# Performance work log

Measured on AMD Instinct MI355X. Metric: run time of the kernel, lower is better.

The kernel has to match this reference:

```python
import jax, jax.numpy as jnp
import numpy as np

LOWER = 300  # hidden size of the critic MLP


def setup_inputs() -> dict:
    key = jax.random.key(0)
    ks = jax.random.split(key, 6)
    N, XD, YD = 1024, 768, 768
    x = jax.random.normal(ks[0], (N, XD), dtype=jnp.float32)
    y = jax.random.normal(ks[1], (N, YD), dtype=jnp.float32)
    # Linear(x_dim+y_dim -> LOWER), Linear(LOWER -> 1); Kaiming-uniform-ish init
    b1_lim = 1.0 / np.sqrt(XD + YD)
    b2_lim = 1.0 / np.sqrt(LOWER)
    W1 = jax.random.uniform(ks[2], (XD + YD, LOWER), jnp.float32, -b1_lim, b1_lim)
    b1 = jax.random.uniform(ks[3], (LOWER,), jnp.float32, -b1_lim, b1_lim)
    W2 = jax.random.uniform(ks[4], (LOWER, 1), jnp.float32, -b2_lim, b2_lim)
    b2 = jax.random.uniform(ks[5], (1,), jnp.float32, -b2_lim, b2_lim)
    return {"x_samples": x, "y_samples": y, "W1": W1, "b1": b1, "W2": W2, "b2": b2}


def reference(x_samples, y_samples, W1, b1, W2, b2):
    N = y_samples.shape[0]
    xd = x_samples.shape[-1]
    # Decompose first Linear: cat([x, y]) @ W1 == x @ W1[:xd] + y @ W1[xd:]
    Wx, Wy = W1[:xd], W1[xd:]
    hx = x_samples @ Wx          # [N, LOWER]
    hy = y_samples @ Wy          # [N, LOWER]
    w2 = W2[:, 0]                # [LOWER]

    def critic(h):
        # relu -> Linear(LOWER->1) -> softplus
        return jax.nn.softplus(jax.nn.relu(h) @ w2 + b2[0])

    # T0[i] = F(x[i], y[i])
    T0 = critic(hx + hy + b1)                       # [N]
    # T1[i, j] = F(x[j], y[i])  (x tiled over dim 0, y over dim 1)
    h_pair = hy[:, None, :] + hx[None, :, :] + b1   # [N, N, LOWER]
    T1 = critic(h_pair)                             # [N, N]
    lower_bound = (T0.mean()
                   - jax.nn.logsumexp(T1, axis=1).mean()
                   - jnp.log(jnp.float32(N)))
    return lower_bound
```

## Files before the change

kernel.cpp:

```cpp
#include <hip/hip_runtime.h>
#include <math.h>

#define N_S 1024
#define XD  768
#define LOW 300
#define KP  320
#define KP2 160

typedef _Float16 h2  __attribute__((ext_vector_type(2)));
typedef __fp16   g2  __attribute__((ext_vector_type(2)));
typedef _Float16 v8h __attribute__((ext_vector_type(8)));
typedef float    f4  __attribute__((ext_vector_type(4)));

union U32H2 { unsigned int u; h2 h; };
__device__ inline h2 u2h(unsigned int v){ U32H2 t; t.u = v; return t.h; }
__device__ inline unsigned int pk(float a, float b){
    g2 t = __builtin_amdgcn_cvt_pkrtz(a, b);
    return __builtin_bit_cast(unsigned int, t);
}
union U4V8 { uint4 u; v8h v; };

__global__ __launch_bounds__(256)
void gemm_h(const float* __restrict__ x, const float* __restrict__ y,
            const float* __restrict__ W1, const float* __restrict__ b1g,
            unsigned int* __restrict__ hx_h, unsigned int* __restrict__ hy_h)
{
    __shared__ unsigned int As[2][32][34];
    __shared__ unsigned int Bs[2][64][34];

    const int tid = threadIdx.x;
    const int job = blockIdx.x;
    const int which = job >= 160;
    const int t = which ? job - 160 : job;
    const int n0 = (t % 5) * 64;
    const int r0 = (t / 5) * 32;
    const float* A = which ? y : x;
    const float* W = W1 + (size_t)which * XD * LOW;
    _Float16* outh = (_Float16*)(which ? hy_h : hx_h);

    const int w = tid >> 6, l = tid & 63;
    const int wn = w & 1, wm = w >> 1;
    const int lr = l & 15, lg = l >> 4;

    const int arow = tid >> 3, aq = tid & 7;
    const int bn = tid & 63, bms = tid >> 6;
    const bool bin = (n0 + bn) < LOW;

    f4 acc[2] = {};
    float4 a0, a1; float bw[16];
    a0 = *(const float4*)&A[(size_t)(r0 + arow) * XD + aq * 8];
    a1 = *(const float4*)&A[(size_t)(r0 + arow) * XD + aq * 8 + 4];
    #pragma unroll
    for (int s = 0; s < 16; ++s)
        bw[s] = bin ? W[(size_t)(bms * 16 + s) * LOW + n0 + bn] : 0.f;

    const int NC = XD / 64;
    for (int c = 0; c < NC; ++c) {
        const int buf = c & 1;
        *(uint4*)&As[buf][arow][aq * 4] =
            uint4{ pk(a0.x,a0.y), pk(a0.z,a0.w), pk(a1.x,a1.y), pk(a1.z,a1.w) };
        *(uint4*)&Bs[buf][bn][bms * 8] =
            uint4{ pk(bw[0],bw[1]), pk(bw[2],bw[3]), pk(bw[4],bw[5]), pk(bw[6],bw[7]) };
        *(uint4*)&Bs[buf][bn][bms * 8 + 4] =
            uint4{ pk(bw[8],bw[9]), pk(bw[10],bw[11]), pk(bw[12],bw[13]), pk(bw[14],bw[15]) };
        __syncthreads();
        if (c + 1 < NC) {
            const int kb = (c + 1) * 64;
            a0 = *(const float4*)&A[(size_t)(r0 + arow) * XD + kb + aq * 8];
            a1 = *(const float4*)&A[(size_t)(r0 + arow) * XD + kb + aq * 8 + 4];
            #pragma unroll
            for (int s = 0; s < 16; ++s)
                bw[s] = bin ? W[(size_t)(kb + bms * 16 + s) * LOW + n0 + bn] : 0.f;
        }
        #pragma unroll
        for (int ks = 0; ks < 2; ++ks) {
            const int ko = ks * 16 + lg * 4;
            U4V8 af; af.u = *(const uint4*)&As[buf][wm * 16 + lr][ko];
            #pragma unroll
            for (int nt = 0; nt < 2; ++nt) {
                U4V8 bf; bf.u = *(const uint4*)&Bs[buf][wn * 32 + nt * 16 + lr][ko];
                acc[nt] = __builtin_amdgcn_mfma_f32_16x16x32_f16(af.v, bf.v, acc[nt], 0, 0, 0);
            }
        }
    }

    #pragma unroll
    for (int nt = 0; nt < 2; ++nt) {
        const int col = n0 + wn * 32 + nt * 16 + lr;
        const float b1v = (which && col < LOW) ? b1g[col] : 0.f;
        #pragma unroll
        for (int r = 0; r < 4; ++r) {
            const int row = r0 + wm * 16 + lg * 4 + r;
            outh[(size_t)row * KP + col] = (_Float16)(acc[nt][r] + b1v);
        }
    }
}

__global__ __launch_bounds__(256)
void pair_kernel(const unsigned int* __restrict__ hx_h, const unsigned int* __restrict__ hy_h,
                 const float* __restrict__ W2, const float* __restrict__ b2,
                 float* __restrict__ part, float* __restrict__ diag)
{
    const int jb = blockIdx.x, ib = blockIdx.y;
    const int j0 = jb * 64, i0 = ib * 32;

    __shared__ unsigned int Hy[160][34];
    __shared__ unsigned int Hx[160][66];
    __shared__ unsigned int w2s[KP2];

    const int tid = threadIdx.x;

    {
        const int r = tid >> 3, q = tid & 7;
        const unsigned int* src = &hy_h[(size_t)(i0 + r) * KP2];
        #pragma unroll
        for (int e = 0; e < 5; ++e) {
            const int k4 = q + 8 * e;
            uint4 v = *(const uint4*)&src[k4 * 4];
            Hy[k4*4+0][r] = v.x; Hy[k4*4+1][r] = v.y;
            Hy[k4*4+2][r] = v.z; Hy[k4*4+3][r] = v.w;
        }
    }
    {
        const int r = tid >> 2, q = tid & 3;
        const unsigned int* src = &hx_h[(size_t)(j0 + r) * KP2];
        #pragma unroll
        for (int e = 0; e < 10; ++e) {
            const int k4 = q + 4 * e;
            uint4 v = *(const uint4*)&src[k4 * 4];
            Hx[k4*4+0][r] = v.x; Hx[k4*4+1][r] = v.y;
            Hx[k4*4+2][r] = v.z; Hx[k4*4+3][r] = v.w;
        }
    }
    if (tid < KP2) {
        int k = tid * 2;
        float w0 = (k < LOW) ? W2[k] : 0.f;
        float w1 = (k + 1 < LOW) ? W2[k + 1] : 0.f;
        w2s[tid] = pk(w0, w1);
    }
    __syncthreads();

    const int tx = tid & 15;
    const int kh = (tid >> 4) & 1;
    const int iy = tid >> 5;

    float acc[4][4] = {};
    const h2 hz = h2{(_Float16)0.f, (_Float16)0.f};
    const int kbase = kh * 80;

    #pragma unroll 4
    for (int kki = 0; kki < 80; ++kki) {
        const int kk = kbase + kki;
        const uint4 ya = *(const uint4*)&Hy[kk][iy * 4];
        const uint4 xb = *(const uint4*)&Hx[kk][tx * 4];
        const h2 w = u2h(w2s[kk]);
        const unsigned int yar[4] = {ya.x, ya.y, ya.z, ya.w};
        const unsigned int xbr[4] = {xb.x, xb.y, xb.z, xb.w};
        #pragma unroll
        for (int r = 0; r < 4; ++r) {
            const h2 a = u2h(yar[r]);
            #pragma unroll
            for (int q = 0; q < 4; ++q) {
                h2 z = __builtin_elementwise_max(a + u2h(xbr[q]), hz);
                acc[r][q] = __builtin_amdgcn_fdot2(z, w, acc[r][q], false);
            }
        }
    }

    #pragma unroll
    for (int r = 0; r < 4; ++r)
        #pragma unroll
        for (int q = 0; q < 4; ++q)
            acc[r][q] += __shfl_xor(acc[r][q], 16, 64);

    const float b2v = b2[0];
    #pragma unroll
    for (int r = 0; r < 4; ++r) {
        const int row = i0 + iy * 4 + r;
        float es = 0.f;
        #pragma unroll
        for (int q = 0; q < 4; ++q) {
            const float s = acc[r][q] + b2v;
            es += __expf(s);
            const int col = j0 + tx * 4 + q;
            if (col == row)
                diag[row] = fmaxf(s, 0.f) + __logf(1.f + __expf(-fabsf(s)));
        }
        #pragma unroll
        for (int o = 1; o <= 8; o <<= 1) es += __shfl_xor(es, o, 64);
        if ((tid & 31) == 0) part[(size_t)row * 16 + jb] = es;
    }
}

__global__ __launch_bounds__(256)
void lse_final(const float* __restrict__ part, const float* __restrict__ diag,
               float* __restrict__ out)
{
    __shared__ float ssum[4];
    const int tid = threadIdx.x;
    float csum = 0.f;
    #pragma unroll
    for (int g = 0; g < 4; ++g) {
        const int row = g * 256 + tid;
        const float4* p = (const float4*)(part + (size_t)row * 16);
        float s = 0.f;
        #pragma unroll
        for (int q = 0; q < 4; ++q) {
            float4 v = p[q];
            s += (v.x + v.y) + (v.z + v.w);
        }
        csum += diag[row] - __logf((float)N_S + s);
    }
    #pragma unroll
    for (int o = 32; o > 0; o >>= 1) csum += __shfl_xor(csum, o, 64);
    if ((tid & 63) == 0) ssum[tid >> 6] = csum;
    __syncthreads();
    if (tid == 0)
        out[0] = (ssum[0] + ssum[1] + ssum[2] + ssum[3]) * (1.0f / N_S)
               - logf((float)N_S);
}

extern "C" void kernel_launch(void* const* d_in, const int* in_sizes, int n_in,
                              void* d_out, int out_size, void* d_ws, size_t ws_size,
                              hipStream_t stream)
{
    const float* x  = (const float*)d_in[0];
    const float* y  = (const float*)d_in[1];
    const float* W1 = (const float*)d_in[2];
    const float* b1 = (const float*)d_in[3];
    const float* W2 = (const float*)d_in[4];
    const float* b2 = (const float*)d_in[5];
    float* outp = (float*)d_out;

    unsigned int* hx_h = (unsigned int*)d_ws;
    unsigned int* hy_h = hx_h + (size_t)N_S * KP2;
    float* part = (float*)(hy_h + (size_t)N_S * KP2);
    float* diag = part + (size_t)N_S * 16;

    gemm_h<<<320, 256, 0, stream>>>(x, y, W1, b1, hx_h, hy_h);

    dim3 g2(16, 32);
    pair_kernel<<<g2, 256, 0, stream>>>(hx_h, hy_h, W2, b2, part, diag);

    lse_final<<<1, 256, 0, stream>>>(part, diag, outp);
}
```

Measured before the change: 40.78 us.

## Fold final reduction into pair kernel and widen GEMM blocks to 512 threads

```diff
diff --git a/kernel.cpp b/kernel.cpp
--- a/kernel.cpp
+++ b/kernel.cpp
@@ -20,16 +20,19 @@
 }
 union U4V8 { uint4 u; v8h v; };
 
-__global__ __launch_bounds__(256)
+__global__ __launch_bounds__(512)
 void gemm_h(const float* __restrict__ x, const float* __restrict__ y,
             const float* __restrict__ W1, const float* __restrict__ b1g,
-            unsigned int* __restrict__ hx_h, unsigned int* __restrict__ hy_h)
+            unsigned int* __restrict__ hx_h, unsigned int* __restrict__ hy_h,
+            unsigned int* __restrict__ cnt)
 {
     __shared__ unsigned int As[2][32][34];
     __shared__ unsigned int Bs[2][64][34];
 
     const int tid = threadIdx.x;
     const int job = blockIdx.x;
+    if (job == 0 && tid == 0) cnt[0] = 0;
+
     const int which = job >= 160;
     const int t = which ? job - 160 : job;
     const int n0 = (t % 5) * 64;
@@ -39,74 +42,65 @@
     _Float16* outh = (_Float16*)(which ? hy_h : hx_h);
 
     const int w = tid >> 6, l = tid & 63;
-    const int wn = w & 1, wm = w >> 1;
+    const int wm = w >> 2, wn = w & 3;
     const int lr = l & 15, lg = l >> 4;
 
-    const int arow = tid >> 3, aq = tid & 7;
+    const int arow = tid >> 4, aq = tid & 15;
     const int bn = tid & 63, bms = tid >> 6;
     const bool bin = (n0 + bn) < LOW;
 
-    f4 acc[2] = {};
-    float4 a0, a1; float bw[16];
-    a0 = *(const float4*)&A[(size_t)(r0 + arow) * XD + aq * 8];
-    a1 = *(const float4*)&A[(size_t)(r0 + arow) * XD + aq * 8 + 4];
-    #pragma unroll
-    for (int s = 0; s < 16; ++s)
-        bw[s] = bin ? W[(size_t)(bms * 16 + s) * LOW + n0 + bn] : 0.f;
+    f4 acc = {};
+    float4 a0; float bw[8];
+    a0 = *(const float4*)&A[(size_t)(r0 + arow) * XD + aq * 4];
+    #pragma unroll
+    for (int s = 0; s < 8; ++s)
+        bw[s] = bin ? W[(size_t)(bms * 8 + s) * LOW + n0 + bn] : 0.f;
 
     const int NC = XD / 64;
     for (int c = 0; c < NC; ++c) {
         const int buf = c & 1;
-        *(uint4*)&As[buf][arow][aq * 4] =
-            uint4{ pk(a0.x,a0.y), pk(a0.z,a0.w), pk(a1.x,a1.y), pk(a1.z,a1.w) };
-        *(uint4*)&Bs[buf][bn][bms * 8] =
+        *(uint2*)&As[buf][arow][aq * 2] = make_uint2(pk(a0.x, a0.y), pk(a0.z, a0.w));
+        *(uint4*)&Bs[buf][bn][bms * 4] =
             uint4{ pk(bw[0],bw[1]), pk(bw[2],bw[3]), pk(bw[4],bw[5]), pk(bw[6],bw[7]) };
-        *(uint4*)&Bs[buf][bn][bms * 8 + 4] =
-            uint4{ pk(bw[8],bw[9]), pk(bw[10],bw[11]), pk(bw[12],bw[13]), pk(bw[14],bw[15]) };
         __syncthreads();
         if (c + 1 < NC) {
             const int kb = (c + 1) * 64;
-            a0 = *(const float4*)&A[(size_t)(r0 + arow) * XD + kb + aq * 8];
-            a1 = *(const float4*)&A[(size_t)(r0 + arow) * XD + kb + aq * 8 + 4];
+            a0 = *(const float4*)&A[(size_t)(r0 + arow) * XD + kb + aq * 4];
             #pragma unroll
-            for (int s = 0; s < 16; ++s)
-                bw[s] = bin ? W[(size_t)(kb + bms * 16 + s) * LOW + n0 + bn] : 0.f;
+            for (int s = 0; s < 8; ++s)
+                bw[s] = bin ? W[(size_t)(kb + bms * 8 + s) * LOW + n0 + bn] : 0.f;
         }
         #pragma unroll
         for (int ks = 0; ks < 2; ++ks) {
             const int ko = ks * 16 + lg * 4;
             U4V8 af; af.u = *(const uint4*)&As[buf][wm * 16 + lr][ko];
-            #pragma unroll
-            for (int nt = 0; nt < 2; ++nt) {
-                U4V8 bf; bf.u = *(const uint4*)&Bs[buf][wn * 32 + nt * 16 + lr][ko];
-                acc[nt] = __builtin_amdgcn_mfma_f32_16x16x32_f16(af.v, bf.v, acc[nt], 0, 0, 0);
-            }
-        }
-    }
-
-    #pragma unroll
-    for (int nt = 0; nt < 2; ++nt) {
-        const int col = n0 + wn * 32 + nt * 16 + lr;
-        const float b1v = (which && col < LOW) ? b1g[col] : 0.f;
-        #pragma unroll
-        for (int r = 0; r < 4; ++r) {
-            const int row = r0 + wm * 16 + lg * 4 + r;
-            outh[(size_t)row * KP + col] = (_Float16)(acc[nt][r] + b1v);
-        }
+            U4V8 bf; bf.u = *(const uint4*)&Bs[buf][wn * 16 + lr][ko];
+            acc = __builtin_amdgcn_mfma_f32_16x16x32_f16(af.v, bf.v, acc, 0, 0, 0);
+        }
+    }
+
+    const int col = n0 + wn * 16 + lr;
+    const float b1v = (which && col < LOW) ? b1g[col] : 0.f;
+    #pragma unroll
+    for (int r = 0; r < 4; ++r) {
+        const int row = r0 + wm * 16 + lg * 4 + r;
+        outh[(size_t)row * KP + col] = (_Float16)(acc[r] + b1v);
     }
 }
 
 __global__ __launch_bounds__(256)
 void pair_kernel(const unsigned int* __restrict__ hx_h, const unsigned int* __restrict__ hy_h,
                  const float* __restrict__ W2, const float* __restrict__ b2,
-                 float* __restrict__ part, float* __restrict__ diag)
+                 float* __restrict__ part, float* __restrict__ diag,
+                 unsigned int* __restrict__ cnt, float* __restrict__ out)
 {
-    const int jb = blockIdx.x, ib = blockIdx.y;
+    const int jb = blockIdx.x & 15, ib = blockIdx.x >> 4;
     const int j0 = jb * 64, i0 = ib * 32;
 
     __shared__ unsigned int Hy[160][34];
     __shared__ unsigned int Hx[160][66];
     __shared__ unsigned int w2s[KP2];
+    __shared__ unsigned int lastFlag;
 
     const int tid = threadIdx.x;
 
@@ -190,14 +184,14 @@
         for (int o = 1; o <= 8; o <<= 1) es += __shfl_xor(es, o, 64);
         if ((tid & 31) == 0) part[(size_t)row * 16 + jb] = es;
     }
-}
-
-__global__ __launch_bounds__(256)
-void lse_final(const float* __restrict__ part, const float* __restrict__ diag,
-               float* __restrict__ out)
-{
+
+    __threadfence();
+    if (tid == 0) lastFlag = (atomicAdd(cnt, 1u) == 511u);
+    __syncthreads();
+    if (!lastFlag) return;
+    __threadfence();
+
     __shared__ float ssum[4];
-    const int tid = threadIdx.x;
     float csum = 0.f;
     #pragma unroll
     for (int g = 0; g < 4; ++g) {
@@ -236,11 +230,10 @@
     unsigned int* hy_h = hx_h + (size_t)N_S * KP2;
     float* part = (float*)(hy_h + (size_t)N_S * KP2);
     float* diag = part + (size_t)N_S * 16;
-
-    gemm_h<<<320, 256, 0, stream>>>(x, y, W1, b1, hx_h, hy_h);
-
-    dim3 g2(16, 32);
-    pair_kernel<<<g2, 256, 0, stream>>>(hx_h, hy_h, W2, b2, part, diag);
-
-    lse_final<<<1, 256, 0, stream>>>(part, diag, outp);
-}
+    unsigned int* cnt = (unsigned int*)(diag + N_S);
+
+    gemm_h<<<320, 512, 0, stream>>>(x, y, W1, b1, hx_h, hy_h, cnt);
+
+    pair_kernel<<<512, 256, 0, stream>>>(hx_h, hy_h, W2, b2, part, diag,
+                                         cnt, outp);
+}
```

Result: slower. 67.38 us (+65.3%).
